# Optimization experiments

Measured on AMD Instinct MI355X. Metric: run time of the kernel, lower is better.

The kernel has to match this reference:

```python
import jax, jax.numpy as jnp
import numpy as np

MIN_NORM = 1e-15
BALL_EPS = 4e-3  # HGCN PoincareBall fp32 boundary eps
C = 1.0          # curvature (init kwarg c)
CLAMP = 1e6      # torch.clamp bound in HypAgg.forward


def _artanh(x):
    # torch Artanh clamps input into open (-1, 1); use fp32-safe eps
    return jnp.arctanh(jnp.clip(x, -1.0 + 1e-7, 1.0 - 1e-7))


def _norm(x):
    return jnp.maximum(jnp.linalg.norm(x, axis=-1, keepdims=True), MIN_NORM)


def mobius_add(x, y, c):
    x2 = jnp.sum(x * x, axis=-1, keepdims=True)
    y2 = jnp.sum(y * y, axis=-1, keepdims=True)
    xy = jnp.sum(x * y, axis=-1, keepdims=True)
    num = (1.0 + 2.0 * c * xy + c * y2) * x + (1.0 - c * x2) * y
    den = 1.0 + 2.0 * c * xy + (c * c) * x2 * y2
    return num / jnp.maximum(den, MIN_NORM)


def lambda_x(x, c):
    return 2.0 / jnp.maximum(1.0 - c * jnp.sum(x * x, axis=-1, keepdims=True), MIN_NORM)


def logmap(p1, p2, c):
    # log_{p1}(p2) on the Poincare ball
    sub = mobius_add(-p1, p2, c)
    sub_norm = _norm(sub)
    sqrt_c = c ** 0.5
    return (2.0 / sqrt_c / lambda_x(p1, c)) * _artanh(sqrt_c * sub_norm) * sub / sub_norm


def expmap(u, p, c):
    sqrt_c = c ** 0.5
    u_norm = _norm(u)
    second = jnp.tanh(sqrt_c / 2.0 * lambda_x(p, c) * u_norm) * u / (sqrt_c * u_norm)
    return mobius_add(p, second, c)


def proj(x, c):
    norm = _norm(x)
    maxnorm = (1.0 - BALL_EPS) / (c ** 0.5)
    return jnp.where(norm > maxnorm, x / norm * maxnorm, x)


def setup_inputs() -> dict:
    key = jax.random.key(0)
    kx, ka, kw = jax.random.split(key, 3)
    B, N, D = 2, 768, 64
    # points strictly inside the unit ball
    x = proj(0.2 * jax.random.normal(kx, (B, N, D), dtype=jnp.float32), C)
    adj = (jax.random.uniform(ka, (B, N, N), dtype=jnp.float32) < 0.05).astype(jnp.float32)
    att_W = jax.random.normal(kw, (2 * D, 1), dtype=jnp.float32) * (1.0 / np.sqrt(2 * D))
    att_b = jnp.zeros((1,), dtype=jnp.float32)
    return {"x": x, "adj": adj, "att_W": att_W, "att_b": att_b}


def reference(x, adj, att_W, att_b):
    c = C
    b, n, d = x.shape
    # pairwise tangent vectors: x_local[b,i,j] = log_{x_i}(x_j)   (b,n,n,d)
    x_i = x[:, :, None, :]
    x_j = x[:, None, :, :]
    x_local = logmap(x_i, x_j, c)
    # log_x(x) == 0 tangent, kept for faithfulness
    x_self = logmap(x, x, c)  # (b,n,d), ~0
    # DenseAtt: linear(2d->1) on [self_tangent || pairwise_tangent], sigmoid, masked by adj
    feats = jnp.concatenate(
        [jnp.broadcast_to(x_self[:, :, None, :], x_local.shape), x_local], axis=-1
    )  # (b,n,n,2d)
    logits = jnp.einsum('bijk,ko->bijo', feats, att_W)[..., 0] + att_b[0]  # (b,n,n)
    att = jax.nn.sigmoid(logits) * adj
    # attention-weighted tangent aggregation over neighbors j
    support_t = jnp.einsum('bij,bijd->bid', att, x_local)
    # proj_tan is identity on the Poincare ball
    support_t = jnp.clip(support_t, -CLAMP, CLAMP)
    return proj(expmap(support_t, x, c), c)
```

## Files before the change

kernel.cpp:

```cpp
#include <hip/hip_runtime.h>
#include <math.h>

#define NB 2
#define NN 768
#define ND 64
#define XSTRIDE 68

__device__ __forceinline__ float fmul_(float a, float b) { float r = a * b; asm volatile("" : "+v"(r)); return r; }
__device__ __forceinline__ float fadd_(float a, float b) { float r = a + b; asm volatile("" : "+v"(r)); return r; }

template <typename F>
__device__ __forceinline__ float pw64(F f) {
  float r[8];
#pragma unroll
  for (int m = 0; m < 8; ++m) r[m] = f(m);
#pragma unroll
  for (int i = 1; i < 8; ++i) {
#pragma unroll
    for (int m = 0; m < 8; ++m) r[m] = fadd_(r[m], f(8 * i + m));
  }
  const float s01 = fadd_(r[0], r[1]), s23 = fadd_(r[2], r[3]);
  const float s45 = fadd_(r[4], r[5]), s67 = fadd_(r[6], r[7]);
  return fadd_(fadd_(s01, s23), fadd_(s45, s67));
}

__device__ __forceinline__ float pwShfl(float v, int lane) {
  const int m = lane & 7;
  float s = __shfl(v, m);
#pragma unroll
  for (int i = 1; i < 8; ++i) s = fadd_(s, __shfl(v, m + 8 * i));
  s = fadd_(s, __shfl_xor(s, 1));
  s = fadd_(s, __shfl_xor(s, 2));
  s = fadd_(s, __shfl_xor(s, 4));
  return s;
}

__device__ __forceinline__ void pwShfl2(float va, float vb, int lane,
                                        float& sa, float& sb) {
  const int m = lane & 7;
  float a = __shfl(va, m), b = __shfl(vb, m);
#pragma unroll
  for (int i = 1; i < 8; ++i) {
    a = fadd_(a, __shfl(va, m + 8 * i));
    b = fadd_(b, __shfl(vb, m + 8 * i));
  }
  a = fadd_(a, __shfl_xor(a, 1)); b = fadd_(b, __shfl_xor(b, 1));
  a = fadd_(a, __shfl_xor(a, 2)); b = fadd_(b, __shfl_xor(b, 2));
  a = fadd_(a, __shfl_xor(a, 4)); b = fadd_(b, __shfl_xor(b, 4));
  sa = a; sb = b;
}

__device__ __forceinline__ float div_rn(float n, float d, float r) {
  const float q0 = n * r;
  const float e  = __builtin_fmaf(-d, q0, n);
  return __builtin_fmaf(e, r, q0);
}

__global__ __launch_bounds__(64) void k_main(const float* __restrict__ x,
                                             const float* __restrict__ adj,
                                             const float* __restrict__ attW,
                                             const float* __restrict__ attb,
                                             float* __restrict__ out) {
  __shared__ float xi_s[ND];
  __shared__ float sW2[ND];
  __shared__ short lj[NN];
  __shared__ float lds_x[64 * XSTRIDE];

  const int row  = blockIdx.x;
  const int b    = row / NN;
  const int lane = threadIdx.x;

  const float xiv = x[(size_t)row * ND + lane];
  xi_s[lane] = xiv;
  sW2[lane]  = attW[ND + lane];

  const float* __restrict__ arow = adj + (size_t)row * NN;
  float av[NN / 64];
#pragma unroll
  for (int c = 0; c < NN / 64; ++c) av[c] = arow[c * 64 + lane];

  const float ni = pwShfl(fmul_(xiv, xiv), lane);

  const float b1  = 1.0f - ni;
  const float lam = 2.0f / fmaxf(b1, 1e-15f);
  const float g1  = 2.0f / lam;
  const float ab  = attb[0];
  const float ATH_CLIP = (float)(1.0 - 1e-07);

  int count = 0, qb1 = 0, qb2 = 0, qb3 = 0;
#pragma unroll
  for (int c = 0; c < NN / 64; ++c) {
    const unsigned long long m = __ballot(av[c] != 0.0f);
    if (av[c] != 0.0f) {
      const int rank = __popcll(m & ((1ull << lane) - 1ull));
      lj[count + rank] = (short)(c * 64 + lane);
    }
    count += __popcll(m);
    if (c == 2) qb1 = count;
    if (c == 5) qb2 = count;
    if (c == 8) qb3 = count;
  }
  __syncthreads();

  const float* __restrict__ xb = x + (size_t)b * NN * ND;
  float pP = 0.0f;
  float Q0 = 0.0f, Q1 = 0.0f, Q2 = 0.0f, Q3 = 0.0f;
  float cfv = 0.0f;

  for (int base = 0; base < count; base += 64) {
    const int valid = min(count - base, 64);

    if (lane < valid) {
      const int j = lj[base + lane];
      float rj[ND];
      const float4* __restrict__ xj4 = (const float4*)(xb + (size_t)j * ND);
#pragma unroll
      for (int k4 = 0; k4 < 16; ++k4) {
        const float4 v = xj4[k4];
        rj[4 * k4 + 0] = v.x; rj[4 * k4 + 1] = v.y;
        rj[4 * k4 + 2] = v.z; rj[4 * k4 + 3] = v.w;
      }
      {
        float4* __restrict__ dst = (float4*)&lds_x[lane * XSTRIDE];
#pragma unroll
        for (int k4 = 0; k4 < 16; ++k4)
          dst[k4] = make_float4(rj[4 * k4], rj[4 * k4 + 1],
                                rj[4 * k4 + 2], rj[4 * k4 + 3]);
      }
      const float nj = pw64([&](int k) { return fmul_(rj[k], rj[k]); });
      const float d  = pw64([&](int k) { return fmul_(xi_s[k], rj[k]); });
      const float xy = -d;
      const float t1  = fadd_(1.0f, 2.0f * xy);
      const float a1  = fadd_(t1, nj);
      const float den = fadd_(t1, fmul_(ni, nj));
      const float denc = fmaxf(den, 1e-15f);
      const float rden = 1.0f / denc;
      float racc[8];
      float subW = 0.0f;
#pragma unroll
      for (int m = 0; m < 8; ++m) {
        const float nk = fadd_(-fmul_(a1, xi_s[m]), fmul_(b1, rj[m]));
        const float sk = div_rn(nk, denc, rden);
        subW = __builtin_fmaf(sk, sW2[m], subW);
        racc[m] = fmul_(sk, sk);
      }
#pragma unroll
      for (int i8 = 1; i8 < 8; ++i8) {
#pragma unroll
        for (int m = 0; m < 8; ++m) {
          const int k = 8 * i8 + m;
          const float nk = fadd_(-fmul_(a1, xi_s[k]), fmul_(b1, rj[k]));
          const float sk = div_rn(nk, denc, rden);
          subW = __builtin_fmaf(sk, sW2[k], subW);
          racc[m] = fadd_(racc[m], fmul_(sk, sk));
        }
      }
      const float s01 = fadd_(racc[0], racc[1]), s23 = fadd_(racc[2], racc[3]);
      const float s45 = fadd_(racc[4], racc[5]), s67 = fadd_(racc[6], racc[7]);
      const float s2  = fadd_(fadd_(s01, s23), fadd_(s45, s67));
      const float t   = sqrtf(s2);
      const float sn  = fmaxf(t, 1e-15f);
      const float z   = fminf(sn, ATH_CLIP);
      const float ath = atanhf(z);
      const float g2  = fmul_(g1, ath);
      const float gg  = g2 / sn;
      const float logit = gg * subW + ab;
      const float sig   = 1.0f / (1.0f + expf(-logit));
      const float cfac  = sig * gg * rden;
      cfv = cfac;
      pP = __builtin_fmaf(cfac, a1, pP);
    }
    __syncthreads();

    const int lim = base + valid;
    {
      const int lo = max(0,   base), hi = min(qb1, lim);
      for (int p2 = lo; p2 < hi; ++p2)
        Q0 = __builtin_fmaf(__shfl(cfv, p2 - base),
                            lds_x[(p2 - base) * XSTRIDE + lane], Q0);
    }
    {
      const int lo = max(qb1, base), hi = min(qb2, lim);
      for (int p2 = lo; p2 < hi; ++p2)
        Q1 = __builtin_fmaf(__shfl(cfv, p2 - base),
                            lds_x[(p2 - base) * XSTRIDE + lane], Q1);
    }
    {
      const int lo = max(qb2, base), hi = min(qb3, lim);
      for (int p2 = lo; p2 < hi; ++p2)
        Q2 = __builtin_fmaf(__shfl(cfv, p2 - base),
                            lds_x[(p2 - base) * XSTRIDE + lane], Q2);
    }
    {
      const int lo = max(qb3, base), hi = min(count, lim);
      for (int p2 = lo; p2 < hi; ++p2)
        Q3 = __builtin_fmaf(__shfl(cfv, p2 - base),
                            lds_x[(p2 - base) * XSTRIDE + lane], Q3);
    }
    __syncthreads();
  }

  float pw = pP;
#pragma unroll
  for (int m = 32; m >= 1; m >>= 1) pw += __shfl_xor(pw, m, 64);
  const float P = pw;
  const float Q = (Q0 + Q1) + (Q2 + Q3);

  float u = b1 * Q - P * xiv;
  u = fminf(fmaxf(u, -1e6f), 1e6f);
  const float u2 = pwShfl(fmul_(u, u), lane);
  const float un = fmaxf(sqrtf(u2), 1e-15f);
  const float th = tanhf(fmul_(0.5f * lam, un));
  const float sec = fmul_(th, u) / un;
  float y2, xys;
  pwShfl2(fmul_(sec, sec), fmul_(xiv, sec), lane, y2, xys);
  const float t1e  = fadd_(1.0f, 2.0f * xys);
  const float a1e  = fadd_(t1e, y2);
  const float dene = fmaxf(fadd_(t1e, fmul_(ni, y2)), 1e-15f);
  const float o    = fadd_(fmul_(a1e, xiv), fmul_(b1, sec)) / dene;
  const float o2 = pwShfl(fmul_(o, o), lane);
  const float nm = fmaxf(sqrtf(o2), 1e-15f);
  const float res = (nm > 0.996f) ? fmul_(o / nm, 0.996f) : o;
  out[(size_t)row * ND + lane] = res;
}

extern "C" void kernel_launch(void* const* d_in, const int* in_sizes, int n_in,
                              void* d_out, int out_size, void* d_ws, size_t ws_size,
                              hipStream_t stream) {
  const float* x    = (const float*)d_in[0];
  const float* adj  = (const float*)d_in[1];
  const float* attW = (const float*)d_in[2];
  const float* attb = (const float*)d_in[3];
  float* out = (float*)d_out;

  hipLaunchKernelGGL(k_main, dim3(NB * NN), dim3(64), 0, stream,
                     x, adj, attW, attb, out);
}
```

Measured before the change: 74.52 us.

## Split each row's neighbors across four waves per block and reduce via LDS

Blocks grow from one to four wavefronts. Neighbor slots are interleaved across the waves, so each lane handles about a quarter as many neighbors and the serial per-lane pairwise work gets shorter. The aggregation loop is also split across waves, and partial P/Q sums are then combined through shared memory before wave 0 runs the expmap/proj epilogue. In exchange, every wave redundantly loads the adjacency row and builds the compaction list, and the change adds an extra barrier plus LDS traffic. Lower lane utilization with ~38 neighbors per row may also increase register pressure at 256 threads.

```diff
diff --git a/kernel.cpp b/kernel.cpp
--- a/kernel.cpp
+++ b/kernel.cpp
@@ -56,23 +56,26 @@
   return __builtin_fmaf(e, r, q0);
 }
 
-__global__ __launch_bounds__(64) void k_main(const float* __restrict__ x,
-                                             const float* __restrict__ adj,
-                                             const float* __restrict__ attW,
-                                             const float* __restrict__ attb,
-                                             float* __restrict__ out) {
+__global__ __launch_bounds__(256) void k_main(const float* __restrict__ x,
+                                              const float* __restrict__ adj,
+                                              const float* __restrict__ attW,
+                                              const float* __restrict__ attb,
+                                              float* __restrict__ out) {
   __shared__ float xi_s[ND];
   __shared__ float sW2[ND];
   __shared__ short lj[NN];
   __shared__ float lds_x[64 * XSTRIDE];
+  __shared__ float qs[4][4][ND];
+  __shared__ float sP[4];
 
   const int row  = blockIdx.x;
   const int b    = row / NN;
-  const int lane = threadIdx.x;
+  const int tid  = threadIdx.x;
+  const int wv   = tid >> 6;
+  const int lane = tid & 63;
 
   const float xiv = x[(size_t)row * ND + lane];
-  xi_s[lane] = xiv;
-  sW2[lane]  = attW[ND + lane];
+  if (wv == 0) { xi_s[lane] = xiv; sW2[lane] = attW[ND + lane]; }
 
   const float* __restrict__ arow = adj + (size_t)row * NN;
   float av[NN / 64];
@@ -109,9 +112,10 @@
 
   for (int base = 0; base < count; base += 64) {
     const int valid = min(count - base, 64);
-
-    if (lane < valid) {
-      const int j = lj[base + lane];
+    const int slot  = 4 * lane + wv;
+
+    if (slot < valid) {
+      const int j = lj[base + slot];
       float rj[ND];
       const float4* __restrict__ xj4 = (const float4*)(xb + (size_t)j * ND);
 #pragma unroll
@@ -121,7 +125,7 @@
         rj[4 * k4 + 2] = v.z; rj[4 * k4 + 3] = v.w;
       }
       {
-        float4* __restrict__ dst = (float4*)&lds_x[lane * XSTRIDE];
+        float4* __restrict__ dst = (float4*)&lds_x[slot * XSTRIDE];
 #pragma unroll
         for (int k4 = 0; k4 < 16; ++k4)
           dst[k4] = make_float4(rj[4 * k4], rj[4 * k4 + 1],
@@ -172,30 +176,14 @@
     }
     __syncthreads();
 
-    const int lim = base + valid;
-    {
-      const int lo = max(0,   base), hi = min(qb1, lim);
-      for (int p2 = lo; p2 < hi; ++p2)
-        Q0 = __builtin_fmaf(__shfl(cfv, p2 - base),
-                            lds_x[(p2 - base) * XSTRIDE + lane], Q0);
-    }
-    {
-      const int lo = max(qb1, base), hi = min(qb2, lim);
-      for (int p2 = lo; p2 < hi; ++p2)
-        Q1 = __builtin_fmaf(__shfl(cfv, p2 - base),
-                            lds_x[(p2 - base) * XSTRIDE + lane], Q1);
-    }
-    {
-      const int lo = max(qb2, base), hi = min(qb3, lim);
-      for (int p2 = lo; p2 < hi; ++p2)
-        Q2 = __builtin_fmaf(__shfl(cfv, p2 - base),
-                            lds_x[(p2 - base) * XSTRIDE + lane], Q2);
-    }
-    {
-      const int lo = max(qb3, base), hi = min(count, lim);
-      for (int p2 = lo; p2 < hi; ++p2)
-        Q3 = __builtin_fmaf(__shfl(cfv, p2 - base),
-                            lds_x[(p2 - base) * XSTRIDE + lane], Q3);
+    for (int s = wv; s < valid; s += 4) {
+      const float cf = __shfl(cfv, s >> 2);
+      const float v  = lds_x[s * XSTRIDE + lane];
+      const int   p2 = base + s;
+      if (p2 < qb1)      Q0 = __builtin_fmaf(cf, v, Q0);
+      else if (p2 < qb2) Q1 = __builtin_fmaf(cf, v, Q1);
+      else if (p2 < qb3) Q2 = __builtin_fmaf(cf, v, Q2);
+      else               Q3 = __builtin_fmaf(cf, v, Q3);
     }
     __syncthreads();
   }
@@ -203,25 +191,40 @@
   float pw = pP;
 #pragma unroll
   for (int m = 32; m >= 1; m >>= 1) pw += __shfl_xor(pw, m, 64);
-  const float P = pw;
-  const float Q = (Q0 + Q1) + (Q2 + Q3);
-
-  float u = b1 * Q - P * xiv;
-  u = fminf(fmaxf(u, -1e6f), 1e6f);
-  const float u2 = pwShfl(fmul_(u, u), lane);
-  const float un = fmaxf(sqrtf(u2), 1e-15f);
-  const float th = tanhf(fmul_(0.5f * lam, un));
-  const float sec = fmul_(th, u) / un;
-  float y2, xys;
-  pwShfl2(fmul_(sec, sec), fmul_(xiv, sec), lane, y2, xys);
-  const float t1e  = fadd_(1.0f, 2.0f * xys);
-  const float a1e  = fadd_(t1e, y2);
-  const float dene = fmaxf(fadd_(t1e, fmul_(ni, y2)), 1e-15f);
-  const float o    = fadd_(fmul_(a1e, xiv), fmul_(b1, sec)) / dene;
-  const float o2 = pwShfl(fmul_(o, o), lane);
-  const float nm = fmaxf(sqrtf(o2), 1e-15f);
-  const float res = (nm > 0.996f) ? fmul_(o / nm, 0.996f) : o;
-  out[(size_t)row * ND + lane] = res;
+  if (lane == 0) sP[wv] = pw;
+  qs[wv][0][lane] = Q0; qs[wv][1][lane] = Q1;
+  qs[wv][2][lane] = Q2; qs[wv][3][lane] = Q3;
+  __syncthreads();
+
+  if (wv == 0) {
+    const float P = fadd_(fadd_(sP[0], sP[1]), fadd_(sP[2], sP[3]));
+    const float q0 = fadd_(fadd_(qs[0][0][lane], qs[1][0][lane]),
+                           fadd_(qs[2][0][lane], qs[3][0][lane]));
+    const float q1 = fadd_(fadd_(qs[0][1][lane], qs[1][1][lane]),
+                           fadd_(qs[2][1][lane], qs[3][1][lane]));
+    const float q2 = fadd_(fadd_(qs[0][2][lane], qs[1][2][lane]),
+                           fadd_(qs[2][2][lane], qs[3][2][lane]));
+    const float q3 = fadd_(fadd_(qs[0][3][lane], qs[1][3][lane]),
+                           fadd_(qs[2][3][lane], qs[3][3][lane]));
+    const float Q = (q0 + q1) + (q2 + q3);
+
+    float u = b1 * Q - P * xiv;
+    u = fminf(fmaxf(u, -1e6f), 1e6f);
+    const float u2 = pwShfl(fmul_(u, u), lane);
+    const float un = fmaxf(sqrtf(u2), 1e-15f);
+    const float th = tanhf(fmul_(0.5f * lam, un));
+    const float sec = fmul_(th, u) / un;
+    float y2, xys;
+    pwShfl2(fmul_(sec, sec), fmul_(xiv, sec), lane, y2, xys);
+    const float t1e  = fadd_(1.0f, 2.0f * xys);
+    const float a1e  = fadd_(t1e, y2);
+    const float dene = fmaxf(fadd_(t1e, fmul_(ni, y2)), 1e-15f);
+    const float o    = fadd_(fmul_(a1e, xiv), fmul_(b1, sec)) / dene;
+    const float o2 = pwShfl(fmul_(o, o), lane);
+    const float nm = fmaxf(sqrtf(o2), 1e-15f);
+    const float res = (nm > 0.996f) ? fmul_(o / nm, 0.996f) : o;
+    out[(size_t)row * ND + lane] = res;
+  }
 }
 
 extern "C" void kernel_launch(void* const* d_in, const int* in_sizes, int n_in,
@@ -233,6 +236,6 @@
   const float* attb = (const float*)d_in[3];
   float* out = (float*)d_out;
 
-  hipLaunchKernelGGL(k_main, dim3(NB * NN), dim3(64), 0, stream,
+  hipLaunchKernelGGL(k_main, dim3(NB * NN), dim3(256), 0, stream,
                      x, adj, attW, attb, out);
 }
```

After: 85.58 us. +14.8%, slower.
